# Kernel optimization log

Hardware: AMD Instinct MI355X
Metric: run time of the kernel (lower is better)

Reference implementation:

```python
import jax, jax.numpy as jnp
import numpy as np

B, T, D, H = 2, 1024, 1024, 16
HS = D // H
EPS = 1e-5
SCALE = float(np.sqrt(HS))  # faithful bug: scores / hs**(-0.5) == scores * sqrt(hs)


def setup_inputs() -> dict:
    key = jax.random.key(0)
    ks = jax.random.split(key, 20)
    n = lambda k, shape: jax.random.normal(k, shape, dtype=jnp.float32) * 0.02
    return {
        "src": jax.random.normal(ks[0], (B, T, D), dtype=jnp.float32),
        "att": jax.random.normal(ks[1], (B, T, D), dtype=jnp.float32),
        # causal masked self-attention (no biases on q/k/v)
        "wq_m": n(ks[2], (H, D, HS)), "wk_m": n(ks[3], (H, D, HS)), "wv_m": n(ks[4], (H, D, HS)),
        "proj_m_w": n(ks[5], (D, D)), "proj_m_b": jnp.zeros((D,), jnp.float32),
        # final (cross) attention (biases on q/k/v)
        "wq_f": n(ks[6], (H, D, HS)), "wk_f": n(ks[7], (H, D, HS)), "wv_f": n(ks[8], (H, D, HS)),
        "bq_f": jnp.zeros((H, HS), jnp.float32), "bk_f": jnp.zeros((H, HS), jnp.float32),
        "bv_f": jnp.zeros((H, HS), jnp.float32),
        "proj_f_w": n(ks[9], (D, D)), "proj_f_b": jnp.zeros((D,), jnp.float32),
        # FFN
        "w1": n(ks[10], (D, 4 * D)), "b1": jnp.zeros((4 * D,), jnp.float32),
        "w2": n(ks[11], (4 * D, D)), "b2": jnp.zeros((D,), jnp.float32),
        # shared RMSNorm weight (one instance reused at all three sites)
        "norm_w": jnp.ones((D,), jnp.float32),
    }


def rmsnorm(x, w):
    return x * jax.lax.rsqrt(jnp.mean(x * x, axis=-1, keepdims=True) + EPS) * w


def masked_attn(x, wq, wk, wv):
    q = jnp.einsum('btd,hde->bhte', x, wq)
    k = jnp.einsum('btd,hde->bhte', x, wk)
    v = jnp.einsum('btd,hde->bhte', x, wv)
    scores = jnp.einsum('bhte,bhse->bhts', q, k) * SCALE  # [B,H,T,T]
    causal = jnp.tril(jnp.ones((T, T), dtype=bool))
    scores = jnp.where(causal, scores, -jnp.inf)
    a = jax.nn.softmax(scores, axis=-1)
    o = jnp.einsum('bhts,bhse->bhte', a, v)
    return o.transpose(0, 2, 1, 3).reshape(B, T, D)  # concat heads


def final_attn(x, att, wq, bq, wk, bk, wv, bv):
    q = jnp.einsum('btd,hde->bhte', att, wq) + bq[None, :, None, :]
    k = jnp.einsum('btd,hde->bhte', att, wk) + bk[None, :, None, :]
    v = jnp.einsum('btd,hde->bhte', x, wv) + bv[None, :, None, :]
    scores = jnp.einsum('bhte,bhse->bhts', q, k) * SCALE
    a = jax.nn.softmax(scores, axis=-1)
    o = jnp.einsum('bhts,bhse->bhte', a, v)
    return o.transpose(0, 2, 1, 3).reshape(B, T, D)


def reference(src, att, wq_m, wk_m, wv_m, proj_m_w, proj_m_b,
              wq_f, wk_f, wv_f, bq_f, bk_f, bv_f, proj_f_w, proj_f_b,
              w1, b1, w2, b2, norm_w):
    # masked self-attention block
    m = masked_attn(rmsnorm(src, norm_w), wq_m, wk_m, wv_m)
    m_out = src + (m @ proj_m_w + proj_m_b)
    # cross attention block (q/k from norm(att), v from m_out)
    f = final_attn(m_out, rmsnorm(att, norm_w), wq_f, bq_f, wk_f, bk_f, wv_f, bv_f)
    f_out = m_out + (f @ proj_f_w + proj_f_b)
    # FFN block
    h = rmsnorm(f_out, norm_w)
    h = jax.nn.gelu(h @ w1 + b1, approximate=False) @ w2 + b2
    return f_out + h
```

## Files before the change

### kernel.cpp

```cpp
#include <hip/hip_runtime.h>
#include <math.h>

#define BB 2
#define TT 1024
#define DD 1024
#define HH 16
#define HS 64
#define NROWS (BB*TT)

typedef _Float16 f16;
typedef __attribute__((ext_vector_type(8))) _Float16 half8;
typedef __attribute__((ext_vector_type(4))) _Float16 half4;
typedef __attribute__((ext_vector_type(4))) float f32x4;

constexpr float EPS   = 1e-5f;
constexpr float SCALE = 8.0f;

__device__ __forceinline__ void load_lds16(const f16* g, f16* l) {
    __builtin_amdgcn_global_load_lds(
        (const __attribute__((address_space(1))) unsigned int*)g,
        (__attribute__((address_space(3))) unsigned int*)l, 16, 0, 0);
}

__device__ __forceinline__ int xcd_swizzle(int lin, int total) {
    if ((total & 7) == 0) {
        const int chunk = total >> 3;
        lin = (lin & 7) * chunk + (lin >> 3);
    }
    return lin;
}

__global__ __launch_bounds__(256) void rms2_kernel(const float* __restrict__ src,
                                                   const float* __restrict__ att,
                                                   const float* __restrict__ w,
                                                   f16* __restrict__ xn_s,
                                                   f16* __restrict__ xn_a) {
    const int bid = blockIdx.x;
    const int tid = threadIdx.x;
    const int row = bid & (NROWS - 1);
    const float* xr = ((bid < NROWS) ? src : att) + (size_t)row * DD;
    f16* out = ((bid < NROWS) ? xn_s : xn_a) + (size_t)row * DD;

    float4 xv = reinterpret_cast<const float4*>(xr)[tid];
    float ss = xv.x*xv.x + xv.y*xv.y + xv.z*xv.z + xv.w*xv.w;

    __shared__ float red[256];
    red[tid] = ss; __syncthreads();
    for (int s = 128; s > 0; s >>= 1) {
        if (tid < s) red[tid] += red[tid + s];
        __syncthreads();
    }
    const float inv = rsqrtf(red[0] * (1.0f / DD) + EPS);

    float4 wv = reinterpret_cast<const float4*>(w)[tid];
    half4 o;
    o.x = (f16)(xv.x * inv * wv.x);
    o.y = (f16)(xv.y * inv * wv.y);
    o.z = (f16)(xv.z * inv * wv.z);
    o.w = (f16)(xv.w * inv * wv.w);
    *reinterpret_cast<half4*>(&out[tid * 4]) = o;
}

__global__ __launch_bounds__(256) void wtrans_all(
    const float* __restrict__ wq_m, const float* __restrict__ wk_m,
    const float* __restrict__ wv_m, const float* __restrict__ proj_m_w,
    const float* __restrict__ wq_f, const float* __restrict__ wk_f,
    const float* __restrict__ wv_f, const float* __restrict__ proj_f_w,
    const float* __restrict__ w1,   const float* __restrict__ w2,
    f16* __restrict__ wt,
    const float* __restrict__ bq, const float* __restrict__ bk,
    float* __restrict__ biascat)
{
    const int bid = blockIdx.x;
    const int tid = threadIdx.x;
    const size_t M_ = 1024 * 1024;

    if (bid >= 4096) {
        for (int j = tid; j < 5120; j += 256)
            biascat[j] = (j < 3072) ? 0.f : ((j < 4096) ? bq[j - 3072] : bk[j - 4096]);
        return;
    }

    const float* W; f16* Wt; int K, N, lognk, t; bool headw;
    if (bid < 768)       { const int m = bid >> 8;
                           W = (m == 0) ? wq_m : (m == 1) ? wk_m : wv_m;
                           Wt = wt + (size_t)m * M_;
                           K = 1024; N = 1024; lognk = 4; headw = true;  t = bid & 255; }
    else if (bid < 1024) { W = proj_m_w; Wt = wt + 6 * M_;
                           K = 1024; N = 1024; lognk = 4; headw = false; t = bid - 768; }
    else if (bid < 1792) { const int m = (bid - 1024) >> 8;
                           W = (m == 0) ? wq_f : (m == 1) ? wk_f : wv_f;
                           Wt = wt + (size_t)(3 + m) * M_;
                           K = 1024; N = 1024; lognk = 4; headw = true;  t = (bid - 1024) & 255; }
    else if (bid < 2048) { W = proj_f_w; Wt = wt + 7 * M_;
                           K = 1024; N = 1024; lognk = 4; headw = false; t = bid - 1792; }
    else if (bid < 3072) { W = w1; Wt = wt + 8 * M_;
                           K = 1024; N = 4096; lognk = 4; headw = false; t = bid - 2048; }
    else                 { W = w2; Wt = wt + 12 * M_;
                           K = 4096; N = 1024; lognk = 6; headw = false; t = bid - 3072; }

    const int k0 = (t & ((1 << lognk) - 1)) * 64;
    const int n0 = (t >> lognk) * 64;

    __shared__ float tt[64][65];
    #pragma unroll
    for (int r = 0; r < 4; ++r) {
        const int idx = tid + r * 256;
        const int kl  = idx >> 4;
        const int nl4 = (idx & 15) * 4;
        const float* gp;
        if (headw) {
            gp = W + ((size_t)(n0 >> 6) * K + (k0 + kl)) * 64 + nl4;
        } else {
            gp = W + (size_t)(k0 + kl) * N + n0 + nl4;
        }
        float4 v = *reinterpret_cast<const float4*>(gp);
        tt[kl][nl4 + 0] = v.x; tt[kl][nl4 + 1] = v.y;
        tt[kl][nl4 + 2] = v.z; tt[kl][nl4 + 3] = v.w;
    }
    __syncthreads();
    #pragma unroll
    for (int r = 0; r < 4; ++r) {
        const int idx = tid + r * 256;
        const int nl  = idx >> 4;
        const int kl4 = (idx & 15) * 4;
        half4 o;
        o.x = (f16)tt[kl4 + 0][nl];
        o.y = (f16)tt[kl4 + 1][nl];
        o.z = (f16)tt[kl4 + 2][nl];
        o.w = (f16)tt[kl4 + 3][nl];
        *reinterpret_cast<half4*>(&Wt[(size_t)(n0 + nl) * K + k0 + kl4]) = o;
    }
}

template<int BM, int EPI, bool HEADOUT, bool SPLITA, bool OHALF, bool PARTIAL>
__global__ __launch_bounds__(256, 2) void gemm_mfma(
    const f16* __restrict__ A1,
    const f16* __restrict__ A2,
    const f16* __restrict__ Bt,
    const float* __restrict__ bias,
    float* __restrict__ outF,
    f16* __restrict__ outH,
    int N, int K, int splitN)
{
    constexpr int BK = 32;
    constexpr int MI = 4;
    constexpr int NI = (BM == 128) ? 4 : 2;
    constexpr int WN = (BM == 128) ? 64 : 32;
    constexpr int ASLOT = BM * 4;
    constexpr int AINST = ASLOT / 256;

    __shared__ f16 ldsA[2][ASLOT * 8];
    __shared__ f16 ldsB[2][512 * 8];

    const int tid  = threadIdx.x;
    const int lane = tid & 63;
    const int wid  = tid >> 6;
    const int gy = gridDim.y;
    const int lin = xcd_swizzle(blockIdx.y * gridDim.x + blockIdx.x,
                                gridDim.x * gy);
    const int m0 = (lin % gy) * BM;
    const int n0 = (lin / gy) * 128;
    const int wm = (BM == 128) ? (wid >> 1) : 0;
    const int wn = (BM == 128) ? (wid & 1) : wid;

    const int Klen  = K / gridDim.z;
    const int kbase = blockIdx.z * Klen;

    const f16* Aptr = (SPLITA && n0 >= splitN) ? A2 : A1;

    f32x4 acc[MI][NI];
    #pragma unroll
    for (int i = 0; i < MI; ++i)
        #pragma unroll
        for (int j = 0; j < NI; ++j)
            acc[i][j] = (f32x4){0.f, 0.f, 0.f, 0.f};

    auto stage = [&](int buf, int kt) {
        const int k0 = kbase + kt * BK;
        #pragma unroll
        for (int i = 0; i < AINST; ++i) {
            const int s   = (wid * AINST + i) * 64 + lane;
            const int kh  = s / BM;
            const int row = s % BM;
            load_lds16(Aptr + (size_t)(m0 + row) * K + (k0 + kh * 8),
                       &ldsA[buf][s * 8]);
        }
        #pragma unroll
        for (int i = 0; i < 2; ++i) {
            const int s   = (wid * 2 + i) * 64 + lane;
            const int kh  = s >> 7;
            const int col = s & 127;
            load_lds16(Bt + (size_t)(n0 + col) * K + (k0 + kh * 8),
                       &ldsB[buf][s * 8]);
        }
    };

    const int NT = Klen / BK;
    stage(0, 0);
    __syncthreads();
    int cur = 0;
    const int l15 = lane & 15, l4 = lane >> 4;
    for (int kt = 0; kt < NT; ++kt) {
        if (kt + 1 < NT) stage(cur ^ 1, kt + 1);
        half8 af[MI], bfr[NI];
        #pragma unroll
        for (int mi = 0; mi < MI; ++mi)
            af[mi] = *reinterpret_cast<const half8*>(
                &ldsA[cur][(l4 * BM + wm * 64 + mi * 16 + l15) * 8]);
        #pragma unroll
        for (int ni = 0; ni < NI; ++ni)
            bfr[ni] = *reinterpret_cast<const half8*>(
                &ldsB[cur][(l4 * 128 + wn * WN + ni * 16 + l15) * 8]);
        #pragma unroll
        for (int mi = 0; mi < MI; ++mi)
            #pragma unroll
            for (int ni = 0; ni < NI; ++ni)
                acc[mi][ni] = __builtin_amdgcn_mfma_f32_16x16x32_f16(
                    af[mi], bfr[ni], acc[mi][ni], 0, 0, 0);
        __syncthreads();
        cur ^= 1;
    }

    f16* pout = nullptr;
    if (PARTIAL) {
        const size_t MN = (size_t)gridDim.y * BM * N;
        pout = outH + (size_t)blockIdx.z * MN;
    }

    #pragma unroll
    for (int mi = 0; mi < MI; ++mi) {
        #pragma unroll
        for (int ni = 0; ni < NI; ++ni) {
            #pragma unroll
            for (int r = 0; r < 4; ++r) {
                const int row = m0 + wm * 64 + mi * 16 + l4 * 4 + r;
                const int col = n0 + wn * WN + ni * 16 + l15;
                float v = acc[mi][ni][r];
                if (PARTIAL) {
                    pout[(size_t)row * N + col] = (f16)v;
                    continue;
                }
                if (EPI >= 1) v += bias[col];
                if (EPI == 2) v = 0.5f * v * (1.0f + erff(v * 0.70710678118f));
                size_t oidx;
                if (HEADOUT) {
                    const int mat = col >> 10;
                    const int h = (col >> 6) & 15, e = col & 63;
                    const int b = row >> 10, t = row & (TT - 1);
                    oidx = (size_t)mat * ((size_t)NROWS * DD)
                         + ((size_t)((b * HH + h) * TT + t)) * HS + e;
                } else {
                    oidx = (size_t)row * N + col;
                }
                if (OHALF) outH[oidx] = (f16)v;
                else       outF[oidx] = v;
            }
        }
    }
}

template<int MODE>
__global__ __launch_bounds__(256) void reduce_fuse(const f16* __restrict__ part,
                                                   const float* __restrict__ bias,
                                                   const float* __restrict__ residF,
                                                   const f16* __restrict__ residH,
                                                   float* __restrict__ outF,
                                                   f16* __restrict__ outH,
                                                   const float* __restrict__ normw,
                                                   f16* __restrict__ xnout) {
    const size_t MN  = (size_t)NROWS * 1024;
    const int tid = threadIdx.x;
    const size_t idx = ((size_t)blockIdx.x * 256 + tid) * 4;
    float o[4];
    {
        half4 p0 = *reinterpret_cast<const half4*>(part + idx);
        half4 p1 = *reinterpret_cast<const half4*>(part + MN + idx);
        half4 p2 = *reinterpret_cast<const half4*>(part + 2 * MN + idx);
        half4 p3 = *reinterpret_cast<const half4*>(part + 3 * MN + idx);
        float4 bi = *reinterpret_cast<const float4*>(bias + (idx & 1023));
        o[0] = (float)p0.x + (float)p1.x + (float)p2.x + (float)p3.x + bi.x;
        o[1] = (float)p0.y + (float)p1.y + (float)p2.y + (float)p3.y + bi.y;
        o[2] = (float)p0.z + (float)p1.z + (float)p2.z + (float)p3.z + bi.z;
        o[3] = (float)p0.w + (float)p1.w + (float)p2.w + (float)p3.w + bi.w;
    }
    if (MODE == 0 || MODE == 2) {
        float4 rs = *reinterpret_cast<const float4*>(residF + idx);
        o[0] += rs.x; o[1] += rs.y; o[2] += rs.z; o[3] += rs.w;
    } else {
        half4 rh = *reinterpret_cast<const half4*>(residH + idx);
        o[0] += (float)rh.x; o[1] += (float)rh.y; o[2] += (float)rh.z; o[3] += (float)rh.w;
    }

    if (MODE == 0) {
        half4 h;
        h.x = (f16)o[0]; h.y = (f16)o[1]; h.z = (f16)o[2]; h.w = (f16)o[3];
        *reinterpret_cast<half4*>(outH + idx) = h;
        return;
    }

    float4 ov = {o[0], o[1], o[2], o[3]};
    *reinterpret_cast<float4*>(outF + idx) = ov;

    if (MODE == 1) {
        __shared__ float red[256];
        red[tid] = o[0]*o[0] + o[1]*o[1] + o[2]*o[2] + o[3]*o[3];
        __syncthreads();
        for (int s = 128; s > 0; s >>= 1) {
            if (tid < s) red[tid] += red[tid + s];
            __syncthreads();
        }
        const float inv = rsqrtf(red[0] * (1.0f / DD) + EPS);
        float4 nw = *reinterpret_cast<const float4*>(normw + (idx & 1023));
        half4 h;
        h.x = (f16)(o[0] * inv * nw.x);
        h.y = (f16)(o[1] * inv * nw.y);
        h.z = (f16)(o[2] * inv * nw.z);
        h.w = (f16)(o[3] * inv * nw.w);
        *reinterpret_cast<half4*>(xnout + idx) = h;
    }
}

template<bool CAUSAL>
__global__ __launch_bounds__(256) void attn_mfma(const f16* __restrict__ Q,
                                                 const f16* __restrict__ Kg,
                                                 const f16* __restrict__ Vg,
                                                 f16* __restrict__ O) {
    const int iq  = blockIdx.x;
    const int bh  = blockIdx.y;
    const int tid = threadIdx.x;
    const int lane = tid & 63;
    const int w   = tid >> 6;
    const int l15 = lane & 15, l4 = lane >> 4;

    __shared__ f16 Ks[512 * 8];
    __shared__ f16 VT[64 * 72];
    __shared__ f16 Ps[4][16 * 72];

    const f16* qb = Q  + ((size_t)bh * TT + (size_t)iq * 64) * HS;
    const f16* kb = Kg + (size_t)bh * TT * HS;
    const f16* vb = Vg + (size_t)bh * TT * HS;

    half8 qf[2];
    #pragma unroll
    for (int ks = 0; ks < 2; ++ks)
        qf[ks] = *reinterpret_cast<const half8*>(
            qb + (size_t)(w * 16 + l15) * HS + ks * 32 + l4 * 8);

    f32x4 oacc[4];
    #pragma unroll
    for (int ni = 0; ni < 4; ++ni) oacc[ni] = (f32x4){0.f, 0.f, 0.f, 0.f};
    float m_run[4], l_run[4];
    #pragma unroll
    for (int r = 0; r < 4; ++r) { m_run[r] = -1e30f; l_run[r] = 0.f; }

    const int sp  = lane & 31;
    const int ehv = lane >> 5;
    const int c0  = w * 16 + ehv * 8;

    const int ntiles = CAUSAL ? (iq + 1) : (TT / 64);
    for (int js = 0; js < ntiles; ++js) {
        __syncthreads();

        #pragma unroll
        for (int i = 0; i < 2; ++i) {
            const int slot = (w * 2 + i) * 64 + lane;
            load_lds16(kb + (size_t)(js * 64 + (slot & 63)) * HS + (slot >> 6) * 8,
                       &Ks[slot * 8]);
        }
        {
            const f16* vrow = vb + (size_t)(js * 64 + 2 * sp) * HS + c0;
            uint4 r0 = *reinterpret_cast<const uint4*>(vrow);
            uint4 r1 = *reinterpret_cast<const uint4*>(vrow + HS);
            const unsigned rc0[4] = {r0.x, r0.y, r0.z, r0.w};
            const unsigned rc1[4] = {r1.x, r1.y, r1.z, r1.w};
            #pragma unroll
            for (int i = 0; i < 8; ++i) {
                const unsigned lo = (i & 1) ? (rc0[i >> 1] >> 16) : (rc0[i >> 1] & 0xffffu);
                const unsigned hi = (i & 1) ? (rc1[i >> 1] >> 16) : (rc1[i >> 1] & 0xffffu);
                *reinterpret_cast<unsigned*>(&VT[(c0 + i) * 72 + 2 * sp]) = lo | (hi << 16);
            }
        }
        __syncthreads();

        f32x4 sacc[4];
        #pragma unroll
        for (int ni = 0; ni < 4; ++ni) sacc[ni] = (f32x4){0.f, 0.f, 0.f, 0.f};
        #pragma unroll
        for (int ks = 0; ks < 2; ++ks) {
            #pragma unroll
            for (int ni = 0; ni < 4; ++ni) {
                half8 kf = *reinterpret_cast<const half8*>(
                    &Ks[((ks * 4 + l4) * 64 + ni * 16 + l15) * 8]);
                sacc[ni] = __builtin_amdgcn_mfma_f32_16x16x32_f16(qf[ks], kf, sacc[ni], 0, 0, 0);
            }
        }

        float sv[4][4];
        #pragma unroll
        for (int ni = 0; ni < 4; ++ni) {
            #pragma unroll
            for (int r = 0; r < 4; ++r) {
                float x = sacc[ni][r] * SCALE;
                if (CAUSAL && js == iq) {
                    const int sg = js * 64 + ni * 16 + l15;
                    const int qg = iq * 64 + w * 16 + l4 * 4 + r;
                    if (sg > qg) x = -1e30f;
                }
                sv[ni][r] = x;
            }
        }

        #pragma unroll
        for (int r = 0; r < 4; ++r) {
            float rm = fmaxf(fmaxf(sv[0][r], sv[1][r]), fmaxf(sv[2][r], sv[3][r]));
            rm = fmaxf(rm, __shfl_xor(rm, 1));
            rm = fmaxf(rm, __shfl_xor(rm, 2));
            rm = fmaxf(rm, __shfl_xor(rm, 4));
            rm = fmaxf(rm, __shfl_xor(rm, 8));
            const float mnew = fmaxf(m_run[r], rm);
            const float corr = __expf(m_run[r] - mnew);
            float p0 = __expf(sv[0][r] - mnew);
            float p1 = __expf(sv[1][r] - mnew);
            float p2 = __expf(sv[2][r] - mnew);
            float p3 = __expf(sv[3][r] - mnew);
            float sum = p0 + p1 + p2 + p3;
            sum += __shfl_xor(sum, 1);
            sum += __shfl_xor(sum, 2);
            sum += __shfl_xor(sum, 4);
            sum += __shfl_xor(sum, 8);
            l_run[r] = l_run[r] * corr + sum;
            m_run[r] = mnew;
            #pragma unroll
            for (int ni = 0; ni < 4; ++ni) oacc[ni][r] *= corr;
            f16* prow = &Ps[w][(l4 * 4 + r) * 72];
            prow[ 0 + l15] = (f16)p0;
            prow[16 + l15] = (f16)p1;
            prow[32 + l15] = (f16)p2;
            prow[48 + l15] = (f16)p3;
        }

        #pragma unroll
        for (int ks = 0; ks < 2; ++ks) {
            half8 pf = *reinterpret_cast<const half8*>(&Ps[w][l15 * 72 + ks * 32 + l4 * 8]);
            #pragma unroll
            for (int ni = 0; ni < 4; ++ni) {
                half8 vf = *reinterpret_cast<const half8*>(
                    &VT[(ni * 16 + l15) * 72 + ks * 32 + l4 * 8]);
                oacc[ni] = __builtin_amdgcn_mfma_f32_16x16x32_f16(pf, vf, oacc[ni], 0, 0, 0);
            }
        }
    }

    const int b = bh >> 4, h = bh & (HH - 1);
    #pragma unroll
    for (int r = 0; r < 4; ++r) {
        const float inv = 1.0f / l_run[r];
        const int t = iq * 64 + w * 16 + l4 * 4 + r;
        #pragma unroll
        for (int ni = 0; ni < 4; ++ni)
            O[((size_t)(b * TT + t)) * DD + h * HS + ni * 16 + l15] =
                (f16)(oacc[ni][r] * inv);
    }
}

extern "C" void kernel_launch(void* const* d_in, const int* in_sizes, int n_in,
                              void* d_out, int out_size, void* d_ws, size_t ws_size,
                              hipStream_t stream) {
    const float* src      = (const float*)d_in[0];
    const float* att      = (const float*)d_in[1];
    const float* wq_m     = (const float*)d_in[2];
    const float* wk_m     = (const float*)d_in[3];
    const float* wv_m     = (const float*)d_in[4];
    const float* proj_m_w = (const float*)d_in[5];
    const float* proj_m_b = (const float*)d_in[6];
    const float* wq_f     = (const float*)d_in[7];
    const float* wk_f     = (const float*)d_in[8];
    const float* wv_f     = (const float*)d_in[9];
    const float* bq_f     = (const float*)d_in[10];
    const float* bk_f     = (const float*)d_in[11];
    const float* bv_f     = (const float*)d_in[12];
    const float* proj_f_w = (const float*)d_in[13];
    const float* proj_f_b = (const float*)d_in[14];
    const float* w1       = (const float*)d_in[15];
    const float* b1       = (const float*)d_in[16];
    const float* w2       = (const float*)d_in[17];
    const float* b2       = (const float*)d_in[18];
    const float* norm_w   = (const float*)d_in[19];

    const size_t M_ = 1024 * 1024;
    f16* wsb = (f16*)d_ws;
    f16* wt      = wsb;
    f16* headbuf = wsb + 16 * M_;
    f16* h1      = wsb + 16 * M_;
    f16* xn_s    = wsb + 28 * M_;
    f16* xn_a    = wsb + 30 * M_;
    f16* ao      = wsb + 32 * M_;
    f16* mo_h    = wsb + 34 * M_;
    f16* partH   = wsb + 36 * M_;
    float* biascat = (float*)d_out;
    float* f_out = (float*)d_out;
    float* outp  = (float*)d_out;
    (void)ws_size; (void)in_sizes; (void)n_in;

    const dim3 blk(256);
    const int BIG = 1 << 30;
    const dim3 gQKV(40, 16);
    const dim3 gVF(8, 32);
    const dim3 gW1(32, 16);
    const dim3 gSPLIT(8, 16, 4);
    const dim3 gRED(2048);

    wtrans_all<<<dim3(4097), blk, 0, stream>>>(
        wq_m, wk_m, wv_m, proj_m_w, wq_f, wk_f, wv_f, proj_f_w, w1, w2,
        wt, bq_f, bk_f, biascat);
    rms2_kernel<<<dim3(2 * NROWS), blk, 0, stream>>>(src, att, norm_w, xn_s, xn_a);

    gemm_mfma<128, 1, true, true, true, false><<<gQKV, blk, 0, stream>>>(
        xn_s, xn_a, wt, biascat, nullptr, headbuf, 5120, 1024, 3072);

    attn_mfma<true><<<dim3(16, 32), blk, 0, stream>>>(
        headbuf, headbuf + 2 * M_, headbuf + 4 * M_, ao);
    gemm_mfma<128, 0, false, false, false, true><<<gSPLIT, blk, 0, stream>>>(
        ao, nullptr, wt + 6 * M_, nullptr, nullptr, partH, 1024, 1024, BIG);
    reduce_fuse<0><<<gRED, blk, 0, stream>>>(
        partH, proj_m_b, src, nullptr, nullptr, mo_h, nullptr, nullptr);

    gemm_mfma<64, 1, true, false, true, false><<<gVF, blk, 0, stream>>>(
        mo_h, nullptr, wt + 5 * M_, bv_f, nullptr, headbuf + 10 * M_, 1024, 1024, BIG);
    attn_mfma<false><<<dim3(16, 32), blk, 0, stream>>>(
        headbuf + 6 * M_, headbuf + 8 * M_, headbuf + 10 * M_, ao);
    gemm_mfma<128, 0, false, false, false, true><<<gSPLIT, blk, 0, stream>>>(
        ao, nullptr, wt + 7 * M_, nullptr, nullptr, partH, 1024, 1024, BIG);
    reduce_fuse<1><<<gRED, blk, 0, stream>>>(
        partH, proj_f_b, nullptr, mo_h, f_out, nullptr, norm_w, xn_s);

    gemm_mfma<128, 2, false, false, true, false><<<gW1, blk, 0, stream>>>(
        xn_s, nullptr, wt + 8 * M_, b1, nullptr, h1, 4096, 1024, BIG);
    gemm_mfma<128, 0, false, false, false, true><<<gSPLIT, blk, 0, stream>>>(
        h1, nullptr, wt + 12 * M_, nullptr, nullptr, partH, 1024, 4096, BIG);
    reduce_fuse<2><<<gRED, blk, 0, stream>>>(
        partH, b2, f_out, nullptr, outp, nullptr, nullptr, nullptr);
}
```

Baseline: 312.2 us.

## Replace syncthreads double-buffer with explicit vmcnt waits and two-stage prefetch

Restructures the GEMM main loop so both LDS buffers are filled up front. Each iteration waits with explicit s_waitcnt vmcnt on only the older stage's direct-to-LDS loads, then uses raw s_barrier instead of __syncthreads. The aim is to keep more global loads in flight and stop draining all outstanding memory ops every K step. The loop is unrolled by two and assumes NT is even. The wait counts are hard-coded to AINST+2 instructions per stage, so they go wrong if the staging layout changes.

```diff
diff --git a/kernel.cpp b/kernel.cpp
--- a/kernel.cpp
+++ b/kernel.cpp
@@ -20,6 +20,14 @@
     __builtin_amdgcn_global_load_lds(
         (const __attribute__((address_space(1))) unsigned int*)g,
         (__attribute__((address_space(3))) unsigned int*)l, 16, 0, 0);
+}
+
+template<int N>
+__device__ __forceinline__ void vm_wait() {
+    if constexpr (N == 0) asm volatile("s_waitcnt vmcnt(0)" ::: "memory");
+    else if constexpr (N == 3) asm volatile("s_waitcnt vmcnt(3)" ::: "memory");
+    else if constexpr (N == 4) asm volatile("s_waitcnt vmcnt(4)" ::: "memory");
+    __builtin_amdgcn_sched_barrier(0);
 }
 
 __device__ __forceinline__ int xcd_swizzle(int lin, int total) {
@@ -149,6 +157,7 @@
     constexpr int WN = (BM == 128) ? 64 : 32;
     constexpr int ASLOT = BM * 4;
     constexpr int AINST = ASLOT / 256;
+    constexpr int STG   = AINST + 2;
 
     __shared__ f16 ldsA[2][ASLOT * 8];
     __shared__ f16 ldsB[2][512 * 8];
@@ -196,30 +205,41 @@
         }
     };
 
-    const int NT = Klen / BK;
-    stage(0, 0);
-    __syncthreads();
-    int cur = 0;
     const int l15 = lane & 15, l4 = lane >> 4;
-    for (int kt = 0; kt < NT; ++kt) {
-        if (kt + 1 < NT) stage(cur ^ 1, kt + 1);
+    auto compute = [&](int buf) {
         half8 af[MI], bfr[NI];
         #pragma unroll
         for (int mi = 0; mi < MI; ++mi)
             af[mi] = *reinterpret_cast<const half8*>(
-                &ldsA[cur][(l4 * BM + wm * 64 + mi * 16 + l15) * 8]);
+                &ldsA[buf][(l4 * BM + wm * 64 + mi * 16 + l15) * 8]);
         #pragma unroll
         for (int ni = 0; ni < NI; ++ni)
             bfr[ni] = *reinterpret_cast<const half8*>(
-                &ldsB[cur][(l4 * 128 + wn * WN + ni * 16 + l15) * 8]);
+                &ldsB[buf][(l4 * 128 + wn * WN + ni * 16 + l15) * 8]);
         #pragma unroll
         for (int mi = 0; mi < MI; ++mi)
             #pragma unroll
             for (int ni = 0; ni < NI; ++ni)
                 acc[mi][ni] = __builtin_amdgcn_mfma_f32_16x16x32_f16(
                     af[mi], bfr[ni], acc[mi][ni], 0, 0, 0);
-        __syncthreads();
-        cur ^= 1;
+    };
+
+    const int NT = Klen / BK;
+    stage(0, 0);
+    stage(1, 1);
+    for (int kt = 0; kt < NT; kt += 2) {
+        vm_wait<STG>();
+        __builtin_amdgcn_s_barrier();
+        compute(0);
+        __builtin_amdgcn_s_barrier();
+        if (kt + 2 < NT) stage(0, kt + 2);
+        if (kt + 2 < NT) vm_wait<STG>(); else vm_wait<0>();
+        __builtin_amdgcn_s_barrier();
+        compute(1);
+        if (kt + 2 < NT) {
+            __builtin_amdgcn_s_barrier();
+            stage(1, kt + 3);
+        }
     }
 
     f16* pout = nullptr;
```

New measurement: 319.3 us. 1.02x slower.
